# Performance work log

Hardware: AMD Instinct MI355X
Metric: run time of the kernel (lower is better)

The kernel has to match this reference:

```python
import jax, jax.numpy as jnp
import numpy as np

B, S, D, H = 1, 2048, 1024, 16
HD = D // H  # head_dim = 64
ROPE_BASE = 10000.0


def setup_inputs() -> dict:
    key = jax.random.key(0)
    k1, k2, k3, k4, k5 = jax.random.split(key, 5)
    std = 0.02
    return {
        "hidden_states": jax.random.normal(k1, (B, S, D), dtype=jnp.float32),
        "attention_mask": jnp.ones((B, S), dtype=jnp.int32),
        "position_ids": jnp.broadcast_to(jnp.arange(S, dtype=jnp.int32), (B, S)),
        "wq": jax.random.normal(k2, (D, D), dtype=jnp.float32) * std,
        "wk": jax.random.normal(k3, (D, D), dtype=jnp.float32) * std,
        "wv": jax.random.normal(k4, (D, D), dtype=jnp.float32) * std,
        "wo": jax.random.normal(k5, (D, D), dtype=jnp.float32) * std,
    }


def _rope_cos_sin(position_ids):
    # standard llama freqs: 1/base^(2i/hd), interleaved-pair rotation
    inv_freq = 1.0 / (ROPE_BASE ** (jnp.arange(0, HD, 2, dtype=jnp.float32) / HD))  # [HD/2]
    freqs = position_ids.astype(jnp.float32)[..., None] * inv_freq  # [B,S,HD/2]
    # add head axis for broadcasting: [B,S,1,HD/2]
    return jnp.cos(freqs)[:, :, None, :], jnp.sin(freqs)[:, :, None, :]


def _apply_rope(x, cos, sin):
    # x: [B,S,H,HD]; pairs (x0,x1) rotated as complex (x0+i*x1)*(cos+i*sin)
    x2 = x.reshape(x.shape[:-1] + (HD // 2, 2))
    x0, x1 = x2[..., 0], x2[..., 1]
    out = jnp.stack([x0 * cos - x1 * sin, x0 * sin + x1 * cos], axis=-1)
    return out.reshape(x.shape)


def _attention(hidden_states, attention_mask, position_ids, wq, wk, wv, wo):
    xq = (hidden_states @ wq).reshape(B, S, H, HD)
    xk = (hidden_states @ wk).reshape(B, S, H, HD)
    xv = (hidden_states @ wv).reshape(B, S, H, HD)

    cos, sin = _rope_cos_sin(position_ids)
    xq = _apply_rope(xq, cos, sin)
    xk = _apply_rope(xk, cos, sin)

    # combined causal + padding mask -> additive bias
    causal = jnp.tril(jnp.ones((S, S), dtype=bool))[None, None]  # [1,1,S,S]
    pad = (attention_mask > 0)[:, None, None, :]  # [B,1,1,S]
    mask = jnp.logical_and(causal, pad)
    neg = jnp.finfo(jnp.float32).min
    bias = jnp.where(mask, 0.0, neg).astype(jnp.float32)

    scale = 1.0 / np.sqrt(HD).astype(np.float32)
    scores = jnp.einsum("bqhd,bkhd->bhqk", xq, xk) * scale + bias  # [B,H,S,S]
    attn_weights = jax.nn.softmax(scores, axis=-1)

    attn_output = jnp.einsum("bhqk,bkhd->bqhd", attn_weights, xv)
    attn_output = attn_output.reshape(B, S, D)
    return attn_output @ wo


def reference(hidden_states, attention_mask, position_ids, wq, wk, wv, wo):
    return _attention(hidden_states, attention_mask, position_ids, wq, wk, wv, wo)
```

## Files before the change

kernel.cpp:

```cpp
#include <hip/hip_runtime.h>
#include <stdint.h>

#define SEQ 2048
#define DMODEL 1024
#define NHEAD 16
#define HDIM 64
#define KCH 128
#define NCHMAX 16
#define NSLOT 544

typedef unsigned short u16;
typedef __attribute__((ext_vector_type(4))) float f32x4;
typedef __attribute__((ext_vector_type(16))) float f32x16;
typedef __attribute__((ext_vector_type(8))) __bf16 bf16x8;
typedef __attribute__((ext_vector_type(8))) u16 u16x8;

__device__ __forceinline__ u16 f2bf(float f) {
  unsigned int u = __builtin_bit_cast(unsigned int, f);
  unsigned int r = (u + 0x7FFFu + ((u >> 16) & 1u)) >> 16;
  return (u16)r;
}
__device__ __forceinline__ float bf2f(u16 b) {
  unsigned int u = ((unsigned int)b) << 16;
  return __builtin_bit_cast(float, u);
}
__device__ __forceinline__ bf16x8 load8(const u16* p) {
  return __builtin_bit_cast(bf16x8, *(const u16x8*)p);
}
__device__ __forceinline__ void gl_lds16(const void* g, void* l) {
  __builtin_amdgcn_global_load_lds(
      (const __attribute__((address_space(1))) unsigned int*)g,
      (__attribute__((address_space(3))) unsigned int*)l, 16, 0, 0);
}

__global__ __launch_bounds__(256) void convert_x(const float* __restrict__ X,
                                                 u16* __restrict__ Xb) {
  int i = (blockIdx.x * 256 + threadIdx.x) * 4;
  float4 v = *(const float4*)(X + i);
  union { u16 s[4]; uint2 u; } o;
  o.s[0] = f2bf(v.x); o.s[1] = f2bf(v.y); o.s[2] = f2bf(v.z); o.s[3] = f2bf(v.w);
  *(uint2*)(Xb + i) = o.u;
}

__global__ __launch_bounds__(256) void transpose_w(
    const float* __restrict__ W0, const float* __restrict__ W1,
    const float* __restrict__ W2, const float* __restrict__ W3,
    u16* __restrict__ T0, u16* __restrict__ T1,
    u16* __restrict__ T2, u16* __restrict__ T3) {
  __shared__ u16 tile[64][65];
  int bz = blockIdx.z;
  const float* W = bz == 0 ? W0 : bz == 1 ? W1 : bz == 2 ? W2 : W3;
  u16* T = bz == 0 ? T0 : bz == 1 ? T1 : bz == 2 ? T2 : T3;
  int n0 = blockIdx.x * 64, k0 = blockIdx.y * 64;
  int t = threadIdx.x;
#pragma unroll 4
  for (int i = 0; i < 16; ++i) {
    int idx = i * 256 + t;
    int r = idx >> 6, c = idx & 63;
    tile[r][c] = f2bf(W[(k0 + r) * 1024 + n0 + c]);
  }
  __syncthreads();
#pragma unroll 4
  for (int i = 0; i < 16; ++i) {
    int idx = i * 256 + t;
    int r = idx >> 6, c = idx & 63;
    T[(n0 + r) * 1024 + k0 + c] = tile[c][r];
  }
}

template <int BM, int BN, int NMATS, bool OUTF32>
__global__ __launch_bounds__(256) void gemm_bf16(
    const u16* __restrict__ A, const u16* __restrict__ B0,
    const u16* __restrict__ B1, const u16* __restrict__ B2,
    u16* __restrict__ O0, u16* __restrict__ O1, u16* __restrict__ O2,
    float* __restrict__ OF) {
  constexpr int MI = BM / 32, NI = BN / 32;
  constexpr int LA = BM / 64, LB = BN / 64;
  __shared__ u16 As[BM * 32];
  __shared__ u16 Bs[BN * 32];
  const int t = threadIdx.x;
  const int lane = t & 63, w = t >> 6;
  const int g = lane >> 4, li = lane & 15;
  const int n0g = blockIdx.x * BN;
  const int mat = n0g >> 10;
  const int n0 = n0g & 1023;
  const u16* Bp = (NMATS == 1 || mat == 0) ? B0 : (mat == 1 ? B1 : B2);
  const int m0 = blockIdx.y * BM;
  const int wm = (w >> 1) * (BM / 2), wn = (w & 1) * (BN / 2);
  f32x4 acc[MI][NI] = {};
  for (int k0 = 0; k0 < 1024; k0 += 32) {
#pragma unroll
    for (int it = 0; it < LA; ++it) {
      int L = it * 2048 + t * 8;
      int r = L >> 5, c = L & 31;
      gl_lds16(A + (m0 + r) * 1024 + k0 + c, (char*)As + it * 4096 + w * 1024);
    }
#pragma unroll
    for (int it = 0; it < LB; ++it) {
      int L = it * 2048 + t * 8;
      int r = L >> 5, c = L & 31;
      gl_lds16(Bp + (n0 + r) * 1024 + k0 + c, (char*)Bs + it * 4096 + w * 1024);
    }
    __syncthreads();
    bf16x8 af[MI], bfr[NI];
#pragma unroll
    for (int mi = 0; mi < MI; ++mi) af[mi] = load8(&As[(wm + mi * 16 + li) * 32 + g * 8]);
#pragma unroll
    for (int ni = 0; ni < NI; ++ni) bfr[ni] = load8(&Bs[(wn + ni * 16 + li) * 32 + g * 8]);
#pragma unroll
    for (int mi = 0; mi < MI; ++mi)
#pragma unroll
      for (int ni = 0; ni < NI; ++ni)
        acc[mi][ni] = __builtin_amdgcn_mfma_f32_16x16x32_bf16(af[mi], bfr[ni], acc[mi][ni], 0, 0, 0);
    __syncthreads();
  }
  u16* Ob = (NMATS == 1 || mat == 0) ? O0 : (mat == 1 ? O1 : O2);
#pragma unroll
  for (int mi = 0; mi < MI; ++mi)
#pragma unroll
    for (int ni = 0; ni < NI; ++ni)
#pragma unroll
      for (int r = 0; r < 4; ++r) {
        int m = m0 + wm + mi * 16 + g * 4 + r;
        int n = n0 + wn + ni * 16 + li;
        float v = acc[mi][ni][r];
        if (OUTF32) OF[m * 1024 + n] = v;
        else Ob[m * 1024 + n] = f2bf(v);
      }
}

__global__ __launch_bounds__(256) void rope_qk(u16* __restrict__ Qb, u16* __restrict__ Kb,
                                               const int* __restrict__ pos_ids) {
  int gid = blockIdx.x * 256 + threadIdx.x;
  int s = gid >> 9;
  int rem = gid & 511;
  int h = rem >> 5, i = rem & 31;
  float pos = (float)pos_ids[s];
  float inv = exp2f(-(float)i * (13.287712379549449f / 32.0f));
  float ang = pos * inv;
  float sn, cs;
  sincosf(ang, &sn, &cs);
  int base = s * 1024 + h * 64 + 2 * i;
  const float qs = 0.125f * 1.4426950408889634f;
  {
    float x0 = bf2f(Qb[base]), x1 = bf2f(Qb[base + 1]);
    Qb[base]     = f2bf((x0 * cs - x1 * sn) * qs);
    Qb[base + 1] = f2bf((x0 * sn + x1 * cs) * qs);
  }
  {
    float x0 = bf2f(Kb[base]), x1 = bf2f(Kb[base + 1]);
    Kb[base]     = f2bf(x0 * cs - x1 * sn);
    Kb[base + 1] = f2bf(x0 * sn + x1 * cs);
  }
}

__global__ __launch_bounds__(256) void v_transpose(const u16* __restrict__ Vb,
                                                   u16* __restrict__ Vt) {
  __shared__ u16 tile[64][65];
  const int t = threadIdx.x;
  const int s0 = blockIdx.x * 64, h = blockIdx.y;
#pragma unroll 4
  for (int i = 0; i < 16; ++i) {
    int idx = i * 256 + t;
    int r = idx >> 6, c = idx & 63;
    tile[r][c] = Vb[(s0 + r) * 1024 + h * 64 + c];
  }
  __syncthreads();
#pragma unroll 4
  for (int i = 0; i < 16; ++i) {
    int idx = i * 256 + t;
    int d = idx >> 6, sc = idx & 63;
    Vt[h * (64 * 2048) + d * 2048 + s0 + sc] = tile[sc][d];
  }
}

__global__ __launch_bounds__(256) void attn_partial(
    const u16* __restrict__ Qb, const u16* __restrict__ Kb,
    const u16* __restrict__ Vt, const int* __restrict__ amask,
    float* __restrict__ Mpart, float* __restrict__ Lpart, u16* __restrict__ Opart) {
  const int t = threadIdx.x, lane = t & 63, w = t >> 6;
  const int l31 = lane & 31;
  const int hi = lane >> 5;
  const int hi4 = hi * 4;
  const int bid = blockIdx.x;
  const int h = bid & 15;
  const int j = (bid >> 4) * 4 + w;
  const int c = (j >= 540) ? 15 : (j >= 532) ? 14 : (j >= 520) ? 13 : (j >= 504) ? 12
              : (j >= 484) ? 11 : (j >= 460) ? 10 : (j >= 432) ? 9 : (j >= 400) ? 8
              : (j >= 364) ? 7 : (j >= 324) ? 6 : (j >= 280) ? 5 : (j >= 232) ? 4
              : (j >= 180) ? 3 : (j >= 124) ? 2 : (j >= 64) ? 1 : 0;
  const int qb = 4 * c + (j - (64 * c - 2 * c * (c - 1)));
  const int q0 = qb * 32;
  const int kstart = c * KCH;
  const int kend = min(kstart + KCH, q0 + 32);
  const u16* Vh = Vt + h * (64 * 2048);
  bf16x8 qf[4];
#pragma unroll
  for (int d16 = 0; d16 < 4; ++d16)
    qf[d16] = load8(Qb + (q0 + l31) * 1024 + h * 64 + d16 * 16 + hi * 8);
  f32x16 acc0 = {}, acc1 = {};
  float m = -1e30f, lsum = 0.f;
  for (int k0 = kstart; k0 < kend; k0 += 32) {
    unsigned int kmsk = (unsigned int)__ballot(amask[k0 + l31] != 0);
    f32x16 s = {};
#pragma unroll
    for (int d16 = 0; d16 < 4; ++d16) {
      bf16x8 kf = load8(Kb + (k0 + l31) * 1024 + h * 64 + d16 * 16 + hi * 8);
      s = __builtin_amdgcn_mfma_f32_32x32x16_bf16(kf, qf[d16], s, 0, 0, 0);
    }
    float sv[16];
    float tmax = -1e30f;
    if (k0 < q0 && kmsk == 0xFFFFFFFFu) {
#pragma unroll
      for (int i = 0; i < 16; ++i) { sv[i] = s[i]; tmax = fmaxf(tmax, s[i]); }
    } else {
      const int qrel = q0 + l31 - k0 - hi4;
      const unsigned int mk = kmsk >> hi4;
#pragma unroll
      for (int i = 0; i < 16; ++i) {
        const int koff = (i & 3) + 8 * (i >> 2);
        bool ok = (((mk >> koff) & 1u) != 0u) && (koff <= qrel);
        float v = ok ? s[i] : -1e30f;
        sv[i] = v;
        tmax = fmaxf(tmax, v);
      }
    }
    float pmax = fmaxf(tmax, __shfl_xor(tmax, 32, 64));
    float mn = fmaxf(m, pmax);
    float alpha = exp2f(m - mn);
    m = mn;
    float p[16];
    float ps = 0.f;
#pragma unroll
    for (int i = 0; i < 16; ++i) { p[i] = exp2f(sv[i] - mn); ps += p[i]; }
    ps += __shfl_xor(ps, 32, 64);
    lsum = lsum * alpha + ps;
    acc0 *= alpha;
    acc1 *= alpha;
    unsigned int pk[8], ot[8];
#pragma unroll
    for (int jj = 0; jj < 8; ++jj)
      pk[jj] = (unsigned int)f2bf(p[2 * jj]) | ((unsigned int)f2bf(p[2 * jj + 1]) << 16);
#pragma unroll
    for (int jj = 0; jj < 8; ++jj) ot[jj] = __shfl_xor(pk[jj], 32, 64);
    union { unsigned int u[4]; bf16x8 v; } f1, f2;
    f1.u[0] = hi ? ot[2] : pk[0];
    f1.u[1] = hi ? ot[3] : pk[1];
    f1.u[2] = hi ? pk[2] : ot[0];
    f1.u[3] = hi ? pk[3] : ot[1];
    f2.u[0] = hi ? ot[6] : pk[4];
    f2.u[1] = hi ? ot[7] : pk[5];
    f2.u[2] = hi ? pk[6] : ot[4];
    f2.u[3] = hi ? pk[7] : ot[5];
    {
      bf16x8 va = load8(Vh + (0 + l31) * 2048 + k0 + hi * 8);
      bf16x8 vb = load8(Vh + (0 + l31) * 2048 + k0 + 16 + hi * 8);
      acc0 = __builtin_amdgcn_mfma_f32_32x32x16_bf16(va, f1.v, acc0, 0, 0, 0);
      acc0 = __builtin_amdgcn_mfma_f32_32x32x16_bf16(vb, f2.v, acc0, 0, 0, 0);
    }
    {
      bf16x8 va = load8(Vh + (32 + l31) * 2048 + k0 + hi * 8);
      bf16x8 vb = load8(Vh + (32 + l31) * 2048 + k0 + 16 + hi * 8);
      acc1 = __builtin_amdgcn_mfma_f32_32x32x16_bf16(va, f1.v, acc1, 0, 0, 0);
      acc1 = __builtin_amdgcn_mfma_f32_32x32x16_bf16(vb, f2.v, acc1, 0, 0, 0);
    }
  }
  const int slot = h * NSLOT + j;
  if (hi == 0) {
    Mpart[slot * 32 + l31] = m;
    Lpart[slot * 32 + l31] = lsum;
  }
  u16* outp = Opart + slot * 2048 + l31 * 64;
#pragma unroll
  for (int grp = 0; grp < 4; ++grp) {
    union { u16 s4[4]; uint2 u; } o0, o1;
#pragma unroll
    for (int r = 0; r < 4; ++r) {
      o0.s4[r] = f2bf(acc0[grp * 4 + r]);
      o1.s4[r] = f2bf(acc1[grp * 4 + r]);
    }
    *(uint2*)(outp + grp * 8 + hi4) = o0.u;
    *(uint2*)(outp + 32 + grp * 8 + hi4) = o1.u;
  }
}

__global__ __launch_bounds__(256) void attn_combine(
    const float* __restrict__ Mpart, const float* __restrict__ Lpart,
    const u16* __restrict__ Opart, u16* __restrict__ Ab) {
  const int qb = blockIdx.x, h = blockIdx.y;
  const int t = threadIdx.x;
  const int q = t >> 3, dg = t & 7;
  const int nch = qb / 4 + 1;
  float M = -1e30f;
#pragma unroll
  for (int c = 0; c < NCHMAX; ++c)
    if (c < nch) {
      int slot = h * NSLOT + (64 * c - 2 * c * (c - 1)) + qb - 4 * c;
      M = fmaxf(M, Mpart[slot * 32 + q]);
    }
  float L = 0.f;
  float o[8] = {};
#pragma unroll
  for (int c = 0; c < NCHMAX; ++c)
    if (c < nch) {
      int slot = h * NSLOT + (64 * c - 2 * c * (c - 1)) + qb - 4 * c;
      float e = exp2f(Mpart[slot * 32 + q] - M);
      L += e * Lpart[slot * 32 + q];
      uint4 pk = *(const uint4*)(Opart + slot * 2048 + q * 64 + dg * 8);
      const u16* ps = (const u16*)&pk;
#pragma unroll
      for (int jj = 0; jj < 8; ++jj) o[jj] += e * bf2f(ps[jj]);
    }
  float inv = 1.f / L;
  u16* dst = Ab + (qb * 32 + q) * 1024 + h * 64 + dg * 8;
  union { u16 s[8]; uint4 u; } ou;
#pragma unroll
  for (int jj = 0; jj < 8; ++jj) ou.s[jj] = f2bf(o[jj] * inv);
  *(uint4*)dst = ou.u;
}

extern "C" void kernel_launch(void* const* d_in, const int* in_sizes, int n_in,
                              void* d_out, int out_size, void* d_ws, size_t ws_size,
                              hipStream_t stream) {
  const float* X = (const float*)d_in[0];
  const int* amask = (const int*)d_in[1];
  const int* pos = (const int*)d_in[2];
  const float* wq = (const float*)d_in[3];
  const float* wk = (const float*)d_in[4];
  const float* wv = (const float*)d_in[5];
  const float* wo = (const float*)d_in[6];
  float* out = (float*)d_out;
  char* ws = (char*)d_ws;
  u16*   Opart = (u16*)(ws);
  u16*   Xb    = (u16*)(ws);
  u16*   Wtq   = (u16*)(ws + (34u << 20));
  u16*   Wtk   = (u16*)(ws + (36u << 20));
  u16*   Wtv   = (u16*)(ws + (38u << 20));
  u16*   Wto   = (u16*)(ws + (40u << 20));
  u16*   Qb    = (u16*)(ws + (42u << 20));
  u16*   Kb    = (u16*)(ws + (46u << 20));
  u16*   Vb    = (u16*)(ws + (50u << 20));
  float* Mpart = (float*)(ws + (50u << 20));
  float* Lpart = (float*)(ws + (51u << 20) + (512u << 10));
  u16*   Vt    = (u16*)(ws + (54u << 20));
  u16*   Ab    = (u16*)(ws + (58u << 20));

  convert_x<<<2048, 256, 0, stream>>>(X, Xb);
  transpose_w<<<dim3(16, 16, 4), 256, 0, stream>>>(wq, wk, wv, wo, Wtq, Wtk, Wtv, Wto);
  gemm_bf16<64, 128, 3, false><<<dim3(24, 32), 256, 0, stream>>>(Xb, Wtq, Wtk, Wtv, Qb, Kb, Vb, nullptr);
  rope_qk<<<4096, 256, 0, stream>>>(Qb, Kb, pos);
  v_transpose<<<dim3(32, 16), 256, 0, stream>>>(Vb, Vt);
  attn_partial<<<2176, 256, 0, stream>>>(Qb, Kb, Vt, amask, Mpart, Lpart, Opart);
  attn_combine<<<dim3(64, 16), 256, 0, stream>>>(Mpart, Lpart, Opart, Ab);
  gemm_bf16<64, 64, 1, true><<<dim3(16, 32), 256, 0, stream>>>(Ab, Wto, nullptr, nullptr,
                                                               nullptr, nullptr, nullptr, out);
}
```

Before: 121.4 us.

## Fuse V transpose into QKV GEMM epilogue and enlarge GEMM tiles with BK=64

The QKV projection GEMM now writes the V output directly in head-major transposed layout (each lane stores 4 consecutive sequence positions as 8 bytes). This removes the separate v_transpose kernel, its launch, and its extra round trip of V through memory. Both GEMMs also gain a BK template parameter: they use a 64-wide K tile with two MFMA substeps per barrier pair, and get larger block tiles (128x128 for QKV, 64x128 for the output projection). That halves the number of synchronisation rounds, at the cost of fewer blocks (384 and 256 respectively), more LDS per block, and strided transposed stores.

```diff
diff --git a/kernel.cpp b/kernel.cpp
--- a/kernel.cpp
+++ b/kernel.cpp
@@ -68,16 +68,17 @@
   }
 }
 
-template <int BM, int BN, int NMATS, bool OUTF32>
+template <int BM, int BN, int BK, int NMATS, bool OUTF32, bool VTOUT>
 __global__ __launch_bounds__(256) void gemm_bf16(
     const u16* __restrict__ A, const u16* __restrict__ B0,
     const u16* __restrict__ B1, const u16* __restrict__ B2,
     u16* __restrict__ O0, u16* __restrict__ O1, u16* __restrict__ O2,
     float* __restrict__ OF) {
   constexpr int MI = BM / 32, NI = BN / 32;
-  constexpr int LA = BM / 64, LB = BN / 64;
-  __shared__ u16 As[BM * 32];
-  __shared__ u16 Bs[BN * 32];
+  constexpr int LA = BM * BK / 2048, LB = BN * BK / 2048;
+  constexpr int KS = BK / 32;
+  __shared__ u16 As[BM * BK];
+  __shared__ u16 Bs[BN * BK];
   const int t = threadIdx.x;
   const int lane = t & 63, w = t >> 6;
   const int g = lane >> 4, li = lane & 15;
@@ -88,45 +89,61 @@
   const int m0 = blockIdx.y * BM;
   const int wm = (w >> 1) * (BM / 2), wn = (w & 1) * (BN / 2);
   f32x4 acc[MI][NI] = {};
-  for (int k0 = 0; k0 < 1024; k0 += 32) {
+  for (int k0 = 0; k0 < 1024; k0 += BK) {
 #pragma unroll
     for (int it = 0; it < LA; ++it) {
       int L = it * 2048 + t * 8;
-      int r = L >> 5, c = L & 31;
+      int r = L / BK, c = L % BK;
       gl_lds16(A + (m0 + r) * 1024 + k0 + c, (char*)As + it * 4096 + w * 1024);
     }
 #pragma unroll
     for (int it = 0; it < LB; ++it) {
       int L = it * 2048 + t * 8;
-      int r = L >> 5, c = L & 31;
+      int r = L / BK, c = L % BK;
       gl_lds16(Bp + (n0 + r) * 1024 + k0 + c, (char*)Bs + it * 4096 + w * 1024);
     }
     __syncthreads();
-    bf16x8 af[MI], bfr[NI];
-#pragma unroll
-    for (int mi = 0; mi < MI; ++mi) af[mi] = load8(&As[(wm + mi * 16 + li) * 32 + g * 8]);
-#pragma unroll
-    for (int ni = 0; ni < NI; ++ni) bfr[ni] = load8(&Bs[(wn + ni * 16 + li) * 32 + g * 8]);
-#pragma unroll
-    for (int mi = 0; mi < MI; ++mi)
+#pragma unroll
+    for (int ks = 0; ks < KS; ++ks) {
+      bf16x8 af[MI], bfr[NI];
+#pragma unroll
+      for (int mi = 0; mi < MI; ++mi)
+        af[mi] = load8(&As[(wm + mi * 16 + li) * BK + ks * 32 + g * 8]);
 #pragma unroll
       for (int ni = 0; ni < NI; ++ni)
-        acc[mi][ni] = __builtin_amdgcn_mfma_f32_16x16x32_bf16(af[mi], bfr[ni], acc[mi][ni], 0, 0, 0);
+        bfr[ni] = load8(&Bs[(wn + ni * 16 + li) * BK + ks * 32 + g * 8]);
+#pragma unroll
+      for (int mi = 0; mi < MI; ++mi)
+#pragma unroll
+        for (int ni = 0; ni < NI; ++ni)
+          acc[mi][ni] = __builtin_amdgcn_mfma_f32_16x16x32_bf16(af[mi], bfr[ni], acc[mi][ni], 0, 0, 0);
+    }
     __syncthreads();
   }
   u16* Ob = (NMATS == 1 || mat == 0) ? O0 : (mat == 1 ? O1 : O2);
 #pragma unroll
   for (int mi = 0; mi < MI; ++mi)
 #pragma unroll
-    for (int ni = 0; ni < NI; ++ni)
-#pragma unroll
-      for (int r = 0; r < 4; ++r) {
-        int m = m0 + wm + mi * 16 + g * 4 + r;
+    for (int ni = 0; ni < NI; ++ni) {
+      if (VTOUT && NMATS == 3 && mat == 2) {
         int n = n0 + wn + ni * 16 + li;
-        float v = acc[mi][ni][r];
-        if (OUTF32) OF[m * 1024 + n] = v;
-        else Ob[m * 1024 + n] = f2bf(v);
+        int hh = n >> 6, dd = n & 63;
+        int sbase = m0 + wm + mi * 16 + g * 4;
+        union { u16 s4[4]; uint2 u; } ov;
+#pragma unroll
+        for (int r = 0; r < 4; ++r) ov.s4[r] = f2bf(acc[mi][ni][r]);
+        *(uint2*)(O2 + hh * (64 * 2048) + dd * 2048 + sbase) = ov.u;
+      } else {
+#pragma unroll
+        for (int r = 0; r < 4; ++r) {
+          int m = m0 + wm + mi * 16 + g * 4 + r;
+          int n = n0 + wn + ni * 16 + li;
+          float v = acc[mi][ni][r];
+          if (OUTF32) OF[m * 1024 + n] = v;
+          else Ob[m * 1024 + n] = f2bf(v);
+        }
       }
+    }
 }
 
 __global__ __launch_bounds__(256) void rope_qk(u16* __restrict__ Qb, u16* __restrict__ Kb,
@@ -151,26 +168,6 @@
     float x0 = bf2f(Kb[base]), x1 = bf2f(Kb[base + 1]);
     Kb[base]     = f2bf(x0 * cs - x1 * sn);
     Kb[base + 1] = f2bf(x0 * sn + x1 * cs);
-  }
-}
-
-__global__ __launch_bounds__(256) void v_transpose(const u16* __restrict__ Vb,
-                                                   u16* __restrict__ Vt) {
-  __shared__ u16 tile[64][65];
-  const int t = threadIdx.x;
-  const int s0 = blockIdx.x * 64, h = blockIdx.y;
-#pragma unroll 4
-  for (int i = 0; i < 16; ++i) {
-    int idx = i * 256 + t;
-    int r = idx >> 6, c = idx & 63;
-    tile[r][c] = Vb[(s0 + r) * 1024 + h * 64 + c];
-  }
-  __syncthreads();
-#pragma unroll 4
-  for (int i = 0; i < 16; ++i) {
-    int idx = i * 256 + t;
-    int d = idx >> 6, sc = idx & 63;
-    Vt[h * (64 * 2048) + d * 2048 + s0 + sc] = tile[sc][d];
   }
 }
 
@@ -339,7 +336,6 @@
   u16*   Wto   = (u16*)(ws + (40u << 20));
   u16*   Qb    = (u16*)(ws + (42u << 20));
   u16*   Kb    = (u16*)(ws + (46u << 20));
-  u16*   Vb    = (u16*)(ws + (50u << 20));
   float* Mpart = (float*)(ws + (50u << 20));
   float* Lpart = (float*)(ws + (51u << 20) + (512u << 10));
   u16*   Vt    = (u16*)(ws + (54u << 20));
@@ -347,11 +343,11 @@
 
   convert_x<<<2048, 256, 0, stream>>>(X, Xb);
   transpose_w<<<dim3(16, 16, 4), 256, 0, stream>>>(wq, wk, wv, wo, Wtq, Wtk, Wtv, Wto);
-  gemm_bf16<64, 128, 3, false><<<dim3(24, 32), 256, 0, stream>>>(Xb, Wtq, Wtk, Wtv, Qb, Kb, Vb, nullptr);
+  gemm_bf16<128, 128, 64, 3, false, true><<<dim3(24, 16), 256, 0, stream>>>(
+      Xb, Wtq, Wtk, Wtv, Qb, Kb, Vt, nullptr);
   rope_qk<<<4096, 256, 0, stream>>>(Qb, Kb, pos);
-  v_transpose<<<dim3(32, 16), 256, 0, stream>>>(Vb, Vt);
   attn_partial<<<2176, 256, 0, stream>>>(Qb, Kb, Vt, amask, Mpart, Lpart, Opart);
   attn_combine<<<dim3(64, 16), 256, 0, stream>>>(Mpart, Lpart, Opart, Ab);
-  gemm_bf16<64, 64, 1, true><<<dim3(16, 32), 256, 0, stream>>>(Ab, Wto, nullptr, nullptr,
-                                                               nullptr, nullptr, nullptr, out);
-}
+  gemm_bf16<64, 128, 64, 1, true, false><<<dim3(8, 32), 256, 0, stream>>>(
+      Ab, Wto, nullptr, nullptr, nullptr, nullptr, nullptr, out);
+}
```

Result: slower. 127.8 us (+5.2%).
